# Kernel tuning notes

Hardware: AMD Instinct MI355X
Metric: run time of the kernel (lower is better)

The kernel has to match this reference:

```python
import jax, jax.numpy as jnp
import numpy as np

EMB_DIM = 768
NUM_HEADS = 12
OUT_DIM = 768


def setup_inputs() -> dict:
    key = jax.random.key(0)
    k_x, k_q, k_k, k_v, k_o = jax.random.split(key, 5)
    B, N, D = 8, 1024, EMB_DIM
    s = 1.0 / np.sqrt(D)
    return {
        "x": jax.random.normal(k_x, (B, N, D), dtype=jnp.float32),
        # torch nn.Linear weights are stored [out_features, in_features]
        "Wq": jax.random.normal(k_q, (D, D), dtype=jnp.float32) * s,
        "Wk": jax.random.normal(k_k, (D, D), dtype=jnp.float32) * s,
        "Wv": jax.random.normal(k_v, (D, D), dtype=jnp.float32) * s,
        "Wo": jax.random.normal(k_o, (OUT_DIM, D), dtype=jnp.float32) * s,
    }


def _split_heads(t, H):
    # [B, N, D] -> [B*H, N, D//H]  (heads folded into batch, per einsum 'b i d')
    B, N, D = t.shape
    return t.reshape(B, N, H, D // H).transpose(0, 2, 1, 3).reshape(B * H, N, D // H)


def _merge_heads(t, B, H):
    BH, N, dh = t.shape
    return t.reshape(B, H, N, dh).transpose(0, 2, 1, 3).reshape(B, N, H * dh)


def reference(x, Wq, Wk, Wv, Wo):
    B, N, D = x.shape
    H = NUM_HEADS
    dh = D // H
    # q/k/v projections (torch Linear: y = x @ W.T, no bias)
    q = _split_heads(x @ Wq.T, H)
    k = _split_heads(x @ Wk.T, H)
    v = _split_heads(x @ Wv.T, H)
    scale = dh ** (-0.5)
    # dots: 'b i d , b j d -> b i j' -> full [B*H, N, N] score matrix
    dots = jnp.einsum('bid,bjd->bij', q, k) * scale
    attn = jax.nn.softmax(dots, axis=-1)
    # dropout p=0.0 -> identity
    # vect: 'b i d , b d j -> b i j' == attn @ v
    vect = jnp.einsum('bij,bjd->bid', attn, v)
    out = _merge_heads(vect, B, H) @ Wo.T
    return out
```

## Files before the change

kernel.cpp:

```cpp
#include <hip/hip_runtime.h>
#include <hip/hip_bf16.h>
#include <stdint.h>


typedef __bf16 bf16x8 __attribute__((ext_vector_type(8)));
typedef __bf16 bf16x4 __attribute__((ext_vector_type(4)));
typedef float f32x4 __attribute__((ext_vector_type(4)));

#define GAS __attribute__((address_space(1)))
#define LAS __attribute__((address_space(3)))

__device__ __forceinline__ void glds16(const short* gp, short* lp) {
  __builtin_amdgcn_global_load_lds((const GAS void*)gp, (LAS void*)lp, 16, 0, 0);
}

__device__ __forceinline__ float fast_exp2(float x) {
#if __has_builtin(__builtin_amdgcn_exp2f)
  return __builtin_amdgcn_exp2f(x);
#else
  return __expf(x * 0.6931471805599453f);
#endif
}

__device__ __forceinline__ short bfbits(float f) {
  __bf16 b = (__bf16)f;
  union { __bf16 b; short s; } cv; cv.b = b;
  return cv.s;
}

__device__ __forceinline__ void stage8_f32(const float* __restrict__ src, short* dst) {
  float4 f0 = ((const float4*)src)[0];
  float4 f1 = ((const float4*)src)[1];
  bf16x8 t;
  t[0] = (__bf16)f0.x; t[1] = (__bf16)f0.y; t[2] = (__bf16)f0.z; t[3] = (__bf16)f0.w;
  t[4] = (__bf16)f1.x; t[5] = (__bf16)f1.y; t[6] = (__bf16)f1.z; t[7] = (__bf16)f1.w;
  *(bf16x8*)dst = t;
}

__global__ __launch_bounds__(256) void convert_kernel(
    const float* __restrict__ x, const float* __restrict__ Wq,
    const float* __restrict__ Wk, const float* __restrict__ Wv,
    const float* __restrict__ Wo,
    short* __restrict__ xb, short* __restrict__ wqkv, short* __restrict__ wob) {
  int u0 = blockIdx.x * 1024 + threadIdx.x;
#pragma unroll
  for (int i = 0; i < 4; ++i) {
    int u = u0 + i * 256;
    const float* src; short* dst;
    if (u < 786432) { src = x + (size_t)u * 8; dst = xb + (size_t)u * 8; }
    else if (u < 1007616) {
      int r = u - 786432;
      int wsel = r / 73728, off = r % 73728;
      const float* W = (wsel == 0) ? Wq : (wsel == 1) ? Wk : Wv;
      src = W + (size_t)off * 8;
      dst = wqkv + (size_t)r * 8;
    } else {
      int r = u - 1007616;
      src = Wo + (size_t)r * 8; dst = wob + (size_t)r * 8;
    }
    stage8_f32(src, dst);
  }
}

__global__ __launch_bounds__(256) void gemm_qkv(
    const short* __restrict__ xb, const short* __restrict__ wqkv,
    short* __restrict__ q, short* __restrict__ k, short* __restrict__ vt) {
  const int m0 = blockIdx.x * 128;
  const int by = blockIdx.y;
  const int n0g = by * 128;
  const int tid = threadIdx.x;
  const int w = tid >> 6, lane = tid & 63, l16 = lane & 15, quad = lane >> 4;
  const int wr = w >> 1, wc = w & 1;

  __shared__ short sA[128 * 64];
  __shared__ short sB[128 * 64];

  f32x4 acc[4][4];
#pragma unroll
  for (int i = 0; i < 4; ++i)
#pragma unroll
    for (int j = 0; j < 4; ++j) acc[i][j] = (f32x4){0.f, 0.f, 0.f, 0.f};

  for (int k0 = 0; k0 < 768; k0 += 64) {
    __syncthreads();
    const short* Ab = xb + (size_t)m0 * 768 + k0;
    const short* Bb = wqkv + (size_t)n0g * 768 + k0;
#pragma unroll
    for (int p = 0; p < 4; ++p) {
      int lin = (w * 4 + p) * 64 + lane;
      int row = lin >> 3;
      int cs = ((lin & 7) ^ (row & 7)) * 8;
      glds16(Ab + (size_t)row * 768 + cs, &sA[lin * 8]);
      glds16(Bb + (size_t)row * 768 + cs, &sB[lin * 8]);
    }
    __syncthreads();
#pragma unroll
    for (int kk2 = 0; kk2 < 2; ++kk2) {
      bf16x8 af[4], bfg[4];
#pragma unroll
      for (int t = 0; t < 4; ++t) {
        int ra = wr * 64 + t * 16 + l16;
        af[t] = *(const bf16x8*)&sA[ra * 64 + (((kk2 * 4 + quad) ^ (ra & 7)) << 3)];
        int rb = wc * 64 + t * 16 + l16;
        bfg[t] = *(const bf16x8*)&sB[rb * 64 + (((kk2 * 4 + quad) ^ (rb & 7)) << 3)];
      }
#pragma unroll
      for (int ti = 0; ti < 4; ++ti)
#pragma unroll
        for (int tj = 0; tj < 4; ++tj)
          acc[ti][tj] = __builtin_amdgcn_mfma_f32_16x16x32_bf16(af[ti], bfg[tj], acc[ti][tj], 0, 0, 0);
    }
  }

  const int wsel = by / 6;
  const int nl0 = (by % 6) * 128 + wc * 64;
  if (wsel == 2) {
#pragma unroll
    for (int ti = 0; ti < 4; ++ti)
#pragma unroll
      for (int tj = 0; tj < 4; ++tj) {
        int token = m0 + wr * 64 + ti * 16 + quad * 4;
        int nl = nl0 + tj * 16 + l16;
        int bh = (token >> 10) * 12 + (nl >> 6);
        short tmp[4];
#pragma unroll
        for (int r = 0; r < 4; ++r) tmp[r] = bfbits(acc[ti][tj][r]);
        *(uint2*)(vt + (size_t)bh * 65536 + (size_t)(nl & 63) * 1024 + (token & 1023)) =
            *(const uint2*)tmp;
      }
  } else {
    short* C = wsel ? k : q;
    const float sc = wsel ? 1.0f : 0.1803368801111244f;
#pragma unroll
    for (int ti = 0; ti < 4; ++ti)
#pragma unroll
      for (int tj = 0; tj < 4; ++tj)
#pragma unroll
        for (int r = 0; r < 4; ++r) {
          int row = m0 + wr * 64 + ti * 16 + quad * 4 + r;
          int nl = nl0 + tj * 16 + l16;
          C[(size_t)row * 768 + nl] = bfbits(acc[ti][tj][r] * sc);
        }
  }
}

__global__ __launch_bounds__(256) void attn_kernel(
    const short* __restrict__ q, const short* __restrict__ k,
    const short* __restrict__ vt, short* __restrict__ vect) {
  const int bh = blockIdx.x % 96;
  const int qt = blockIdx.x / 96;
  const int b = bh / 12, h = bh % 12;
  const int m0 = qt * 64;
  const int tid = threadIdx.x;
  const int w = tid >> 6, lane = tid & 63, l16 = lane & 15, quad = lane >> 4;

  __shared__ short sK[128 * 64];
  __shared__ short sVt[64 * 128];

  const size_t base = (size_t)b * 786432 + (size_t)h * 64;
  const size_t vbase = (size_t)bh * 65536;

#pragma unroll
  for (int p = 0; p < 2; ++p) {
    int lin = (w * 2 + p) * 64 + lane;
    int row = lin >> 3;
    int cs = ((lin & 7) ^ (row & 7)) * 8;
    glds16(q + base + (size_t)(m0 + row) * 768 + cs, &sK[lin * 8]);
  }
  __syncthreads();
  bf16x8 bq[2];
#pragma unroll
  for (int kk = 0; kk < 2; ++kk) {
    int row = w * 16 + l16;
    bq[kk] = *(const bf16x8*)&sK[row * 64 + (((kk * 4 + quad) ^ (row & 7)) << 3)];
  }

  f32x4 l4 = (f32x4){0.f, 0.f, 0.f, 0.f};
  f32x4 oacc[4];
#pragma unroll
  for (int td = 0; td < 4; ++td) oacc[td] = (f32x4){0.f, 0.f, 0.f, 0.f};

  for (int j0 = 0; j0 < 1024; j0 += 128) {
    __syncthreads();
#pragma unroll
    for (int p = 0; p < 4; ++p) {
      int lin = (w * 4 + p) * 64 + lane;
      int row = lin >> 3;
      int cs = ((lin & 7) ^ (row & 7)) * 8;
      glds16(k + base + (size_t)(j0 + row) * 768 + cs, &sK[lin * 8]);
    }
#pragma unroll
    for (int p = 0; p < 4; ++p) {
      int lin = (w * 4 + p) * 64 + lane;
      int row = lin >> 4;
      int c = lin & 15;
      int cs = (c ^ (row & 15)) * 8;
      glds16(vt + vbase + (size_t)row * 1024 + j0 + cs, &sVt[lin * 8]);
    }
    __syncthreads();

#pragma unroll
    for (int jh = 0; jh < 2; ++jh) {
      f32x4 s[4];
#pragma unroll
      for (int ti = 0; ti < 4; ++ti) s[ti] = (f32x4){0.f, 0.f, 0.f, 0.f};
#pragma unroll
      for (int kk = 0; kk < 2; ++kk)
#pragma unroll
        for (int ti = 0; ti < 4; ++ti) {
          int row = jh * 64 + ti * 16 + l16;
          bf16x8 a = *(const bf16x8*)&sK[row * 64 + (((kk * 4 + quad) ^ (row & 7)) << 3)];
          s[ti] = __builtin_amdgcn_mfma_f32_16x16x32_bf16(a, bq[kk], s[ti], 0, 0, 0);
        }

      bf16x4 pb[4];
#pragma unroll
      for (int ti = 0; ti < 4; ++ti) {
        f32x4 e;
        e[0] = fast_exp2(s[ti][0]);
        e[1] = fast_exp2(s[ti][1]);
        e[2] = fast_exp2(s[ti][2]);
        e[3] = fast_exp2(s[ti][3]);
        l4 += e;
        bf16x4 tb;
        tb[0] = (__bf16)e[0]; tb[1] = (__bf16)e[1];
        tb[2] = (__bf16)e[2]; tb[3] = (__bf16)e[3];
        pb[ti] = tb;
      }

#pragma unroll
      for (int t2 = 0; t2 < 2; ++t2) {
        union { bf16x4 hh[2]; bf16x8 v; } bp;
        bp.hh[0] = pb[2 * t2];
        bp.hh[1] = pb[2 * t2 + 1];
#pragma unroll
        for (int td = 0; td < 4; ++td) {
          int row = td * 16 + l16;
          int o1 = jh * 64 + t2 * 32 + quad * 4;
          int c1 = o1 >> 3, w1 = o1 & 7;
          int c2 = c1 + 2;
          union { uint2 u[2]; bf16x8 v; } tmp;
          tmp.u[0] = *(const uint2*)&sVt[row * 128 + ((c1 ^ (row & 15)) << 3) + w1];
          tmp.u[1] = *(const uint2*)&sVt[row * 128 + ((c2 ^ (row & 15)) << 3) + w1];
          oacc[td] = __builtin_amdgcn_mfma_f32_16x16x32_bf16(tmp.v, bp.v, oacc[td], 0, 0, 0);
        }
      }
    }
  }

  float l = (l4[0] + l4[1]) + (l4[2] + l4[3]);
  l += __shfl_xor(l, 16);
  l += __shfl_xor(l, 32);
  float inv = 1.0f / l;
  int i_tok = m0 + w * 16 + l16;
#pragma unroll
  for (int td = 0; td < 4; ++td) {
    short tmp[4];
#pragma unroll
    for (int r = 0; r < 4; ++r) tmp[r] = bfbits(oacc[td][r] * inv);
    *(uint2*)(vect + base + (size_t)i_tok * 768 + td * 16 + quad * 4) = *(const uint2*)tmp;
  }
}

__global__ __launch_bounds__(256) void gemm_out(
    const short* __restrict__ vect, const short* __restrict__ wob,
    float* __restrict__ out) {
  const int m0 = blockIdx.x * 64;
  const int n0 = blockIdx.y * 128;
  const int tid = threadIdx.x;
  const int w = tid >> 6, lane = tid & 63, l16 = lane & 15, quad = lane >> 4;
  const int wr = w >> 1, wc = w & 1;

  __shared__ short sA[64 * 64];
  __shared__ short sB[128 * 64];

  f32x4 acc[2][4];
#pragma unroll
  for (int i = 0; i < 2; ++i)
#pragma unroll
    for (int j = 0; j < 4; ++j) acc[i][j] = (f32x4){0.f, 0.f, 0.f, 0.f};

  for (int k0 = 0; k0 < 768; k0 += 64) {
    __syncthreads();
    const short* Ab = vect + (size_t)m0 * 768 + k0;
    const short* Bb = wob + (size_t)n0 * 768 + k0;
#pragma unroll
    for (int p = 0; p < 2; ++p) {
      int lin = (w * 2 + p) * 64 + lane;
      int row = lin >> 3;
      int cs = ((lin & 7) ^ (row & 7)) * 8;
      glds16(Ab + (size_t)row * 768 + cs, &sA[lin * 8]);
    }
#pragma unroll
    for (int p = 0; p < 4; ++p) {
      int lin = (w * 4 + p) * 64 + lane;
      int row = lin >> 3;
      int cs = ((lin & 7) ^ (row & 7)) * 8;
      glds16(Bb + (size_t)row * 768 + cs, &sB[lin * 8]);
    }
    __syncthreads();
#pragma unroll
    for (int kk2 = 0; kk2 < 2; ++kk2) {
      bf16x8 af[2], bfg[4];
#pragma unroll
      for (int t = 0; t < 2; ++t) {
        int ra = wr * 32 + t * 16 + l16;
        af[t] = *(const bf16x8*)&sA[ra * 64 + (((kk2 * 4 + quad) ^ (ra & 7)) << 3)];
      }
#pragma unroll
      for (int t = 0; t < 4; ++t) {
        int rb = wc * 64 + t * 16 + l16;
        bfg[t] = *(const bf16x8*)&sB[rb * 64 + (((kk2 * 4 + quad) ^ (rb & 7)) << 3)];
      }
#pragma unroll
      for (int ti = 0; ti < 2; ++ti)
#pragma unroll
        for (int tj = 0; tj < 4; ++tj)
          acc[ti][tj] = __builtin_amdgcn_mfma_f32_16x16x32_bf16(af[ti], bfg[tj], acc[ti][tj], 0, 0, 0);
    }
  }
#pragma unroll
  for (int ti = 0; ti < 2; ++ti)
#pragma unroll
    for (int tj = 0; tj < 4; ++tj)
#pragma unroll
      for (int r = 0; r < 4; ++r) {
        int row = m0 + wr * 32 + ti * 16 + quad * 4 + r;
        int col = n0 + wc * 64 + tj * 16 + l16;
        out[(size_t)row * 768 + col] = acc[ti][tj][r];
      }
}

extern "C" void kernel_launch(void* const* d_in, const int* in_sizes, int n_in,
                              void* d_out, int out_size, void* d_ws, size_t ws_size,
                              hipStream_t stream) {
  const float* x  = (const float*)d_in[0];
  const float* Wq = (const float*)d_in[1];
  const float* Wk = (const float*)d_in[2];
  const float* Wv = (const float*)d_in[3];
  const float* Wo = (const float*)d_in[4];
  float* out = (float*)d_out;

  const size_t MN = (size_t)8192 * 768;
  short* q    = (short*)d_ws;
  short* k    = q + MN;
  short* vt   = k + MN;
  short* vect = q;
  short* wob  = vt + MN;

  short* xb   = (short*)d_out;
  short* wqkv = xb + MN;

  convert_kernel<<<1056, 256, 0, stream>>>(x, Wq, Wk, Wv, Wo, xb, wqkv, wob);
  gemm_qkv<<<dim3(64, 18), 256, 0, stream>>>(xb, wqkv, q, k, vt);
  attn_kernel<<<1536, 256, 0, stream>>>(q, k, vt, vect);
  gemm_out<<<dim3(128, 6), 256, 0, stream>>>(vect, wob, out);
}
```

Measured before the change: 194.2 us.

## Rewrite QKV GEMM as 256x256 tiles with double-buffered LDS pipeline

The QKV projection GEMM moves from 128x128 tiles with 256 threads and a load-sync-compute loop to 256x256 tiles with 512 threads. Each tile is split into half-tiles that are double-buffered in LDS, with global-to-LDS prefetch interleaved between MFMA phases and controlled by explicit vmcnt waits and barriers. It also adds s_setprio around the MFMA bursts and a swizzled block order for L2 locality. The aim is to raise arithmetic intensity and hide global load latency. In exchange it uses 128 KB of LDS per block and relies on fragile hand-written wait counts, and the 288-block grid may underfill the GPU.

```diff
diff --git a/kernel.cpp b/kernel.cpp
--- a/kernel.cpp
+++ b/kernel.cpp
@@ -62,85 +62,188 @@
   }
 }
 
-__global__ __launch_bounds__(256) void gemm_qkv(
+__device__ __forceinline__ void stage_half(const short* __restrict__ g, short* l,
+                                           int w, int lane) {
+#pragma unroll
+  for (int p = 0; p < 2; ++p) {
+    int c = (w * 2 + p) * 64 + lane;
+    int row = c >> 3;
+    int cs = ((c & 7) ^ (row & 7)) * 8;
+    glds16(g + (size_t)row * 768 + cs, l + c * 8);
+  }
+}
+
+__device__ __forceinline__ void bar_fence() {
+  asm volatile("" ::: "memory");
+  __builtin_amdgcn_s_barrier();
+  asm volatile("" ::: "memory");
+}
+
+__device__ __forceinline__ void load_a8(const short* base, int wr, int l16, int quad,
+                                        bf16x8 (&fa)[4][2]) {
+#pragma unroll
+  for (int mf = 0; mf < 4; ++mf)
+#pragma unroll
+    for (int kk = 0; kk < 2; ++kk) {
+      int row = wr * 64 + mf * 16 + l16;
+      fa[mf][kk] = *(const bf16x8*)&base[row * 64 + ((((kk << 2) + quad) ^ (row & 7)) << 3)];
+    }
+}
+
+__device__ __forceinline__ void load_b4(const short* base, int rbase, int l16, int quad,
+                                        bf16x8 (&fb)[2][2]) {
+#pragma unroll
+  for (int nf = 0; nf < 2; ++nf)
+#pragma unroll
+    for (int kk = 0; kk < 2; ++kk) {
+      int row = rbase + nf * 16 + l16;
+      fb[nf][kk] = *(const bf16x8*)&base[row * 64 + ((((kk << 2) + quad) ^ (row & 7)) << 3)];
+    }
+}
+
+__device__ __forceinline__ void mma16(const bf16x8 (&fa)[4][2], const bf16x8 (&fb)[2][2],
+                                      f32x4 (&acc)[4][4], int nf0) {
+  __builtin_amdgcn_s_setprio(1);
+#pragma unroll
+  for (int kk = 0; kk < 2; ++kk)
+#pragma unroll
+    for (int mf = 0; mf < 4; ++mf)
+#pragma unroll
+      for (int nf = 0; nf < 2; ++nf)
+        acc[mf][nf0 + nf] = __builtin_amdgcn_mfma_f32_16x16x32_bf16(
+            fa[mf][kk], fb[nf][kk], acc[mf][nf0 + nf], 0, 0, 0);
+  __builtin_amdgcn_s_setprio(0);
+}
+
+__global__ __launch_bounds__(512, 2) void gemm_qkv(
     const short* __restrict__ xb, const short* __restrict__ wqkv,
     short* __restrict__ q, short* __restrict__ k, short* __restrict__ vt) {
-  const int m0 = blockIdx.x * 128;
-  const int by = blockIdx.y;
-  const int n0g = by * 128;
+  const int lin = blockIdx.x;
+  const int swz = (lin & 7) * 36 + (lin >> 3);
+  const int bx = swz & 31;
+  const int by = swz >> 5;
+  const int m0 = bx * 256;
+  const int n0g = by * 256;
   const int tid = threadIdx.x;
   const int w = tid >> 6, lane = tid & 63, l16 = lane & 15, quad = lane >> 4;
-  const int wr = w >> 1, wc = w & 1;
-
-  __shared__ short sA[128 * 64];
-  __shared__ short sB[128 * 64];
-
-  f32x4 acc[4][4];
-#pragma unroll
-  for (int i = 0; i < 4; ++i)
-#pragma unroll
-    for (int j = 0; j < 4; ++j) acc[i][j] = (f32x4){0.f, 0.f, 0.f, 0.f};
-
-  for (int k0 = 0; k0 < 768; k0 += 64) {
-    __syncthreads();
-    const short* Ab = xb + (size_t)m0 * 768 + k0;
-    const short* Bb = wqkv + (size_t)n0g * 768 + k0;
-#pragma unroll
-    for (int p = 0; p < 4; ++p) {
-      int lin = (w * 4 + p) * 64 + lane;
-      int row = lin >> 3;
-      int cs = ((lin & 7) ^ (row & 7)) * 8;
-      glds16(Ab + (size_t)row * 768 + cs, &sA[lin * 8]);
-      glds16(Bb + (size_t)row * 768 + cs, &sB[lin * 8]);
-    }
-    __syncthreads();
-#pragma unroll
-    for (int kk2 = 0; kk2 < 2; ++kk2) {
-      bf16x8 af[4], bfg[4];
-#pragma unroll
-      for (int t = 0; t < 4; ++t) {
-        int ra = wr * 64 + t * 16 + l16;
-        af[t] = *(const bf16x8*)&sA[ra * 64 + (((kk2 * 4 + quad) ^ (ra & 7)) << 3)];
-        int rb = wc * 64 + t * 16 + l16;
-        bfg[t] = *(const bf16x8*)&sB[rb * 64 + (((kk2 * 4 + quad) ^ (rb & 7)) << 3)];
-      }
-#pragma unroll
-      for (int ti = 0; ti < 4; ++ti)
-#pragma unroll
-        for (int tj = 0; tj < 4; ++tj)
-          acc[ti][tj] = __builtin_amdgcn_mfma_f32_16x16x32_bf16(af[ti], bfg[tj], acc[ti][tj], 0, 0, 0);
-    }
-  }
-
-  const int wsel = by / 6;
-  const int nl0 = (by % 6) * 128 + wc * 64;
+  const int wr = w >> 2, wc = w & 3;
+
+  __shared__ short lds[2][2][2][8192];
+
+  const short* Asrc = xb + (size_t)m0 * 768;
+  const short* Bsrc = wqkv + (size_t)n0g * 768;
+
+  f32x4 acc[2][4][4];
+#pragma unroll
+  for (int h = 0; h < 2; ++h)
+#pragma unroll
+    for (int i = 0; i < 4; ++i)
+#pragma unroll
+      for (int j = 0; j < 4; ++j) acc[h][i][j] = (f32x4){0.f, 0.f, 0.f, 0.f};
+
+  stage_half(Asrc, &lds[0][0][0][0], w, lane);
+  stage_half(Bsrc, &lds[0][1][0][0], w, lane);
+  stage_half(Bsrc + 98304, &lds[0][1][1][0], w, lane);
+  stage_half(Asrc + 98304, &lds[0][0][1][0], w, lane);
+  stage_half(Asrc + 64, &lds[1][0][0][0], w, lane);
+  stage_half(Bsrc + 64, &lds[1][1][0][0], w, lane);
+  stage_half(Bsrc + 98304 + 64, &lds[1][1][1][0], w, lane);
+  asm volatile("s_waitcnt vmcnt(6)" ::: "memory");
+  bar_fence();
+
+  const int bh = wc >> 1;
+  const int rb0 = (wc & 1) * 64;
+  const short* bb0 = &lds[0][1][bh][0];
+  const short* bb1 = &lds[1][1][bh][0];
+
+  bf16x8 fa[4][2], fb0[2][2], fb1[2][2];
+
+  for (int i = 0; i < 6; ++i) {
+    const int t1 = 2 * i + 1, t2 = 2 * i + 2, t3 = 2 * i + 3;
+    const bool pf = (i < 5);
+
+    load_a8(&lds[0][0][0][0], wr, l16, quad, fa);
+    load_b4(bb0, rb0, l16, quad, fb0);
+    stage_half(Asrc + 98304 + (size_t)t1 * 64, &lds[1][0][1][0], w, lane);
+    bar_fence();
+    mma16(fa, fb0, acc[0], 0);
+    bar_fence();
+    load_b4(bb0, rb0 + 32, l16, quad, fb1);
+    if (pf) stage_half(Asrc + (size_t)t2 * 64, &lds[0][0][0][0], w, lane);
+    bar_fence();
+    mma16(fa, fb1, acc[0], 2);
+    bar_fence();
+    load_a8(&lds[0][0][1][0], wr, l16, quad, fa);
+    if (pf) stage_half(Bsrc + (size_t)t2 * 64, &lds[0][1][0][0], w, lane);
+    bar_fence();
+    mma16(fa, fb1, acc[1], 2);
+    bar_fence();
+    if (pf) {
+      stage_half(Bsrc + 98304 + (size_t)t2 * 64, &lds[0][1][1][0], w, lane);
+      asm volatile("s_waitcnt vmcnt(6)" ::: "memory");
+    } else {
+      asm volatile("s_waitcnt vmcnt(0)" ::: "memory");
+    }
+    bar_fence();
+    mma16(fa, fb0, acc[1], 0);
+    bar_fence();
+
+    load_a8(&lds[1][0][0][0], wr, l16, quad, fa);
+    load_b4(bb1, rb0, l16, quad, fb0);
+    if (pf) stage_half(Asrc + 98304 + (size_t)t2 * 64, &lds[0][0][1][0], w, lane);
+    bar_fence();
+    mma16(fa, fb0, acc[0], 0);
+    bar_fence();
+    load_b4(bb1, rb0 + 32, l16, quad, fb1);
+    if (pf) stage_half(Asrc + (size_t)t3 * 64, &lds[1][0][0][0], w, lane);
+    bar_fence();
+    mma16(fa, fb1, acc[0], 2);
+    bar_fence();
+    load_a8(&lds[1][0][1][0], wr, l16, quad, fa);
+    if (pf) stage_half(Bsrc + (size_t)t3 * 64, &lds[1][1][0][0], w, lane);
+    bar_fence();
+    mma16(fa, fb1, acc[1], 2);
+    bar_fence();
+    if (pf) stage_half(Bsrc + 98304 + (size_t)t3 * 64, &lds[1][1][1][0], w, lane);
+    asm volatile("s_waitcnt vmcnt(6)" ::: "memory");
+    bar_fence();
+    mma16(fa, fb0, acc[1], 0);
+    bar_fence();
+  }
+
+  const int wsel = by / 3;
+  const int nl0 = (by % 3) * 256 + wc * 64;
   if (wsel == 2) {
 #pragma unroll
-    for (int ti = 0; ti < 4; ++ti)
-#pragma unroll
-      for (int tj = 0; tj < 4; ++tj) {
-        int token = m0 + wr * 64 + ti * 16 + quad * 4;
-        int nl = nl0 + tj * 16 + l16;
-        int bh = (token >> 10) * 12 + (nl >> 6);
-        short tmp[4];
-#pragma unroll
-        for (int r = 0; r < 4; ++r) tmp[r] = bfbits(acc[ti][tj][r]);
-        *(uint2*)(vt + (size_t)bh * 65536 + (size_t)(nl & 63) * 1024 + (token & 1023)) =
-            *(const uint2*)tmp;
-      }
+    for (int h = 0; h < 2; ++h)
+#pragma unroll
+      for (int mf = 0; mf < 4; ++mf)
+#pragma unroll
+        for (int nf = 0; nf < 4; ++nf) {
+          int token = m0 + h * 128 + wr * 64 + mf * 16 + quad * 4;
+          int nl = nl0 + nf * 16 + l16;
+          int bhh = (token >> 10) * 12 + (nl >> 6);
+          short tmp[4];
+#pragma unroll
+          for (int r = 0; r < 4; ++r) tmp[r] = bfbits(acc[h][mf][nf][r]);
+          *(uint2*)(vt + (size_t)bhh * 65536 + (size_t)(nl & 63) * 1024 + (token & 1023)) =
+              *(const uint2*)tmp;
+        }
   } else {
     short* C = wsel ? k : q;
     const float sc = wsel ? 1.0f : 0.1803368801111244f;
 #pragma unroll
-    for (int ti = 0; ti < 4; ++ti)
-#pragma unroll
-      for (int tj = 0; tj < 4; ++tj)
-#pragma unroll
-        for (int r = 0; r < 4; ++r) {
-          int row = m0 + wr * 64 + ti * 16 + quad * 4 + r;
-          int nl = nl0 + tj * 16 + l16;
-          C[(size_t)row * 768 + nl] = bfbits(acc[ti][tj][r] * sc);
-        }
+    for (int h = 0; h < 2; ++h)
+#pragma unroll
+      for (int mf = 0; mf < 4; ++mf)
+#pragma unroll
+        for (int nf = 0; nf < 4; ++nf)
+#pragma unroll
+          for (int r = 0; r < 4; ++r) {
+            int row = m0 + h * 128 + wr * 64 + mf * 16 + quad * 4 + r;
+            int nl = nl0 + nf * 16 + l16;
+            C[(size_t)row * 768 + nl] = bfbits(acc[h][mf][nf][r] * sc);
+          }
   }
 }
 
@@ -352,7 +455,7 @@
   short* wqkv = xb + MN;
 
   convert_kernel<<<1056, 256, 0, stream>>>(x, Wq, Wk, Wv, Wo, xb, wqkv, wob);
-  gemm_qkv<<<dim3(64, 18), 256, 0, stream>>>(xb, wqkv, q, k, vt);
+  gemm_qkv<<<288, 512, 0, stream>>>(xb, wqkv, q, k, vt);
   attn_kernel<<<1536, 256, 0, stream>>>(q, k, vt, vect);
   gemm_out<<<dim3(128, 6), 256, 0, stream>>>(vect, wob, out);
 }
```

New measurement: 200.4 us. 1.03x slower.
